# Performance work log

Measured on AMD Instinct MI355X. Metric: run time of the kernel, lower is better.

## Reference

```python
import jax, jax.numpy as jnp
import numpy as np

D_MODEL = 1536
NUM_EXPERTS = 64
TOP_K = 2
D_HIDDEN = 512
LN_EPS = 1e-5


def setup_inputs() -> dict:
    key = jax.random.key(0)
    ks = jax.random.split(key, 6)
    B, S = 2, 2048
    x = jax.random.normal(ks[0], (B, S, D_MODEL), dtype=jnp.float32)
    # router: nn.Linear(d_model, num_experts, bias=False) -> weight [E, D]
    Wr = jax.random.normal(ks[1], (NUM_EXPERTS, D_MODEL), dtype=jnp.float32) / np.sqrt(D_MODEL)
    # per-expert MLP weights, torch Linear layout: w1 [H, D], w2 [D, H], stacked over experts
    W1 = jax.random.normal(ks[2], (NUM_EXPERTS, D_HIDDEN, D_MODEL), dtype=jnp.float32) / np.sqrt(D_MODEL)
    W2 = jax.random.normal(ks[3], (NUM_EXPERTS, D_MODEL, D_HIDDEN), dtype=jnp.float32) / np.sqrt(D_HIDDEN)
    gamma = jnp.ones((D_MODEL,), dtype=jnp.float32)
    beta = jnp.zeros((D_MODEL,), dtype=jnp.float32)
    return {"x": x, "Wr": Wr, "W1": W1, "W2": W2, "gamma": gamma, "beta": beta}


def reference(x, Wr, W1, W2, gamma, beta):
    B, S, D = x.shape
    xf = x.reshape(-1, D)                                   # [T, D]
    logits = xf @ Wr.T                                      # [T, E]
    top_w, top_idx = jax.lax.top_k(logits, TOP_K)           # [T, K]
    top_w = jax.nn.softmax(top_w, axis=-1)                  # softmax over selected k
    # combine[t, e] = sum_k top_w[t, k] * 1{top_idx[t,k]==e}; zero for unselected experts,
    # so dense all-expert compute below is mathematically identical to the masked loop.
    onehot = jax.nn.one_hot(top_idx, NUM_EXPERTS, dtype=xf.dtype)   # [T, K, E]
    combine = jnp.einsum("tk,tke->te", top_w, onehot)       # [T, E]
    h = jax.nn.silu(jnp.einsum("td,ehd->teh", xf, W1))      # [T, E, H]
    hw = h * combine[:, :, None]                            # weight before second GEMM
    out = jnp.einsum("teh,edh->td", hw, W2)                 # [T, D]
    # LayerNorm (eps=1e-5, affine)
    mu = jnp.mean(out, axis=-1, keepdims=True)
    var = jnp.mean(jnp.square(out - mu), axis=-1, keepdims=True)
    out = (out - mu) * jax.lax.rsqrt(var + LN_EPS) * gamma + beta
    return out.reshape(B, S, D)
```

## Files before the change

### kernel.cpp

```cpp
#include <hip/hip_runtime.h>
#include <hip/hip_bf16.h>

#define D_MODEL 1536
#define NEXP    64
#define D_HID   512
#define NTOK    4096
#define NT1     (D_MODEL / 64)
#define NT2     (D_HID / 64)
#define MT      192

typedef __attribute__((ext_vector_type(8))) short short8;
typedef __attribute__((ext_vector_type(4))) float f32x4;

__device__ __forceinline__ unsigned short f2bf(float f) {
  unsigned u = __builtin_bit_cast(unsigned, f);
  u += 0x7FFFu + ((u >> 16) & 1u);
  return (unsigned short)(u >> 16);
}
__device__ __forceinline__ unsigned pk2(float a, float b) {
  return (unsigned)f2bf(a) | ((unsigned)f2bf(b) << 16);
}
__device__ __forceinline__ float bf2f(unsigned short u) {
  return __builtin_bit_cast(float, ((unsigned)u) << 16);
}

__device__ __forceinline__ void gl16(const void* g, void* s) {
  __builtin_amdgcn_global_load_lds(
      (const __attribute__((address_space(1))) unsigned int*)g,
      (__attribute__((address_space(3))) unsigned int*)s, 16, 0, 0);
}

#define WAITV(N)  asm volatile("s_waitcnt vmcnt(" #N ")" ::: "memory")
#define WAITL0    asm volatile("s_waitcnt lgkmcnt(0)" ::: "memory")
#define SBAR      __builtin_amdgcn_s_barrier()
#define SCHED0    __builtin_amdgcn_sched_barrier(0)


__global__ void zero_small_kernel(int* __restrict__ counts) {
  counts[threadIdx.x] = 0;
}


__global__ __launch_bounds__(256) void cvt_split_kernel(const float* __restrict__ x,
    const float* __restrict__ Wr,
    unsigned short* __restrict__ xhi, unsigned short* __restrict__ xlo,
    unsigned short* __restrict__ whi, unsigned short* __restrict__ wlo)
{
  const float* src; unsigned short* dhi; unsigned short* dlo; long i;
  long bid = blockIdx.x;
  if (bid < 3072) { src = x;  dhi = xhi; dlo = xlo; i = (bid * 256 + threadIdx.x) * 8; }
  else            { src = Wr; dhi = whi; dlo = wlo; i = ((bid - 3072) * 256 + threadIdx.x) * 8; }
  float4 a = *(const float4*)(src + i);
  float4 b = *(const float4*)(src + i + 4);
  float f[8] = {a.x, a.y, a.z, a.w, b.x, b.y, b.z, b.w};
  unsigned short h[8], l[8];
  #pragma unroll
  for (int j = 0; j < 8; ++j) {
    h[j] = f2bf(f[j]);
    l[j] = f2bf(f[j] - bf2f(h[j]));
  }
  uint4 ph, pl;
  ph.x = (unsigned)h[0] | ((unsigned)h[1] << 16);
  ph.y = (unsigned)h[2] | ((unsigned)h[3] << 16);
  ph.z = (unsigned)h[4] | ((unsigned)h[5] << 16);
  ph.w = (unsigned)h[6] | ((unsigned)h[7] << 16);
  pl.x = (unsigned)l[0] | ((unsigned)l[1] << 16);
  pl.y = (unsigned)l[2] | ((unsigned)l[3] << 16);
  pl.z = (unsigned)l[4] | ((unsigned)l[5] << 16);
  pl.w = (unsigned)l[6] | ((unsigned)l[7] << 16);
  *(uint4*)(dhi + i) = ph;
  *(uint4*)(dlo + i) = pl;
}


__global__ __launch_bounds__(256) void router_kernel(
    const unsigned short* __restrict__ xhi, const unsigned short* __restrict__ xlo,
    const unsigned short* __restrict__ whi, const unsigned short* __restrict__ wlo,
    int* __restrict__ topidx, float* __restrict__ topw, int* __restrict__ counts)
{
  __shared__ unsigned short lds[8 * 4096];
  const int tid  = threadIdx.x;
  const int lane = tid & 63;
  const int wv   = tid >> 6;
  const int t0   = blockIdx.x * 64;

  const int lslot = (lane & 7) ^ (lane >> 3);
  const unsigned short* gsrc[4][2];
  #pragma unroll
  for (int j = 0; j < 2; ++j) {
    int r = (wv * 2 + j) * 8 + (lane >> 3);
    gsrc[0][j] = xhi + (long)(t0 + r) * D_MODEL + lslot * 8;
    gsrc[1][j] = xlo + (long)(t0 + r) * D_MODEL + lslot * 8;
    gsrc[2][j] = whi + (long)r * D_MODEL + lslot * 8;
    gsrc[3][j] = wlo + (long)r * D_MODEL + lslot * 8;
  }

  auto ISSUE = [&](int t, int b) {
    const int k0 = t * 64;
    SCHED0;
    #pragma unroll
    for (int tile = 0; tile < 4; ++tile)
      #pragma unroll
      for (int j = 0; j < 2; ++j)
        gl16(gsrc[tile][j] + k0, &lds[(b * 4 + tile) * 4096 + (wv * 2 + j) * 512]);
    SCHED0;
  };

  f32x4 acc[4];
  #pragma unroll
  for (int i = 0; i < 4; ++i) acc[i] = (f32x4)0.f;

  const int arow = wv * 16 + (lane & 15);

  auto COMPUTE = [&](int b) {
    const unsigned short* Ah = &lds[(b * 4 + 0) * 4096];
    const unsigned short* Al = &lds[(b * 4 + 1) * 4096];
    const unsigned short* Bh = &lds[(b * 4 + 2) * 4096];
    const unsigned short* Bl = &lds[(b * 4 + 3) * 4096];
    #pragma unroll
    for (int ks = 0; ks < 2; ++ks) {
      int pa = (ks * 4 + (lane >> 4)) ^ (arow & 7);
      short8 ah = *(const short8*)(Ah + arow * 64 + pa * 8);
      short8 al = *(const short8*)(Al + arow * 64 + pa * 8);
      short8 bh[4], bl[4];
      #pragma unroll
      for (int ni = 0; ni < 4; ++ni) {
        int br = ni * 16 + (lane & 15);
        int pb = (ks * 4 + (lane >> 4)) ^ (br & 7);
        bh[ni] = *(const short8*)(Bh + br * 64 + pb * 8);
        bl[ni] = *(const short8*)(Bl + br * 64 + pb * 8);
      }
      __builtin_amdgcn_s_setprio(1);
      #pragma unroll
      for (int ni = 0; ni < 4; ++ni) {
        acc[ni] = __builtin_amdgcn_mfma_f32_16x16x32_bf16(ah, bh[ni], acc[ni], 0, 0, 0);
        acc[ni] = __builtin_amdgcn_mfma_f32_16x16x32_bf16(ah, bl[ni], acc[ni], 0, 0, 0);
        acc[ni] = __builtin_amdgcn_mfma_f32_16x16x32_bf16(al, bh[ni], acc[ni], 0, 0, 0);
      }
      __builtin_amdgcn_s_setprio(0);
    }
  };

  ISSUE(0, 0);
  ISSUE(1, 1);
  WAITV(8);
  SBAR;

  #pragma unroll 1
  for (int t = 0; t < NT1; t += 2) {
    COMPUTE(0);
    SBAR;
    if (t + 2 < NT1) { ISSUE(t + 2, 0); WAITV(8); }
    else             { WAITV(0); }
    SBAR;
    COMPUTE(1);
    SBAR;
    if (t + 2 < NT1) {
      if (t + 3 < NT1) { ISSUE(t + 3, 1); WAITV(8); }
      else             { WAITV(0); }
      SBAR;
    }
  }

  float* lgl = (float*)lds;
  #pragma unroll
  for (int ni = 0; ni < 4; ++ni)
    #pragma unroll
    for (int rg = 0; rg < 4; ++rg) {
      int tok = wv * 16 + (lane >> 4) * 4 + rg;
      int e   = ni * 16 + (lane & 15);
      lgl[tok * 66 + e] = acc[ni][rg];
    }
  __syncthreads();

  for (int i = 0; i < 16; ++i) {
    const int tl = wv * 16 + i;
    float v = lgl[tl * 66 + lane];
    float v0 = v; int e0 = lane;
    #pragma unroll
    for (int off = 32; off > 0; off >>= 1) {
      float ov = __shfl_xor(v0, off);
      int   oe = __shfl_xor(e0, off);
      if (ov > v0 || (ov == v0 && oe < e0)) { v0 = ov; e0 = oe; }
    }
    float v1 = (lane == e0) ? -3.0e38f : v;
    int e1 = lane;
    #pragma unroll
    for (int off = 32; off > 0; off >>= 1) {
      float ov = __shfl_xor(v1, off);
      int   oe = __shfl_xor(e1, off);
      if (ov > v1 || (ov == v1 && oe < e1)) { v1 = ov; e1 = oe; }
    }
    if (lane == 0) {
      int tt = t0 + tl;
      float w0 = 1.f / (1.f + expf(v1 - v0));
      topidx[tt * 2]     = e0;
      topidx[tt * 2 + 1] = e1;
      topw[tt * 2]       = w0;
      topw[tt * 2 + 1]   = 1.f - w0;
      atomicAdd(&counts[e0], 1);
      atomicAdd(&counts[e1], 1);
    }
  }
}


__global__ void scan_kernel(const int* __restrict__ counts, int* __restrict__ offs,
                            int* __restrict__ cursor)
{
  int e = threadIdx.x;
  int c = counts[e];
  int xx = c;
  #pragma unroll
  for (int off = 1; off < 64; off <<= 1) {
    int y = __shfl_up(xx, off);
    if (e >= off) xx += y;
  }
  offs[e + 1] = xx;
  if (e == 0) offs[0] = 0;
  cursor[e] = 0;
}

__global__ void scatter_kernel(const int* __restrict__ topidx, const float* __restrict__ topw,
    const int* __restrict__ offs, int* __restrict__ cursor,
    int* __restrict__ perm, float* __restrict__ wgt, int* __restrict__ tok2slot)
{
  int t = blockIdx.x * blockDim.x + threadIdx.x;
  if (t >= NTOK) return;
  #pragma unroll
  for (int k = 0; k < 2; ++k) {
    int e = topidx[t * 2 + k];
    float w = topw[t * 2 + k];
    int pos = atomicAdd(&cursor[e], 1);
    int slot = offs[e] + pos;
    perm[slot] = t;
    wgt[slot] = w;
    tok2slot[t * 2 + k] = slot;
  }
}

#define FS(T, AB, BRI, BRW, KNT)                                   \
  {                                                                \
    COMPUTE(Abuf[AB], Bbuf[AB]);                                   \
    SBAR;                                                          \
    if ((T) + 2 < (KNT)) ISSUEA((T) + 2, Abuf[AB]);                \
    if ((T) + 3 < (KNT)) ISSUEB((T) + 3, BRI);                     \
    if ((T) + 3 < (KNT))      { WAITV(14); }                       \
    else if ((T) + 2 < (KNT)) { WAITV(10); }                       \
    else                      { WAITV(0);  }                       \
    if ((T) + 1 < (KNT)) { WRITE_B(BRW, Bbuf[(AB) ^ 1]); WAITL0; } \
    SBAR;                                                          \
  }


__global__ __launch_bounds__(256, 2) void ffn1_kernel(
    const unsigned short* __restrict__ xb, const float* __restrict__ W1,
    const int* __restrict__ offs, const int* __restrict__ perm,
    const float* __restrict__ wgt, unsigned short* __restrict__ hbuf)
{
  const int bid = blockIdx.x;
  const int e   = (bid & 7) * 8 + (bid >> 6);
  const int nc  = (bid >> 3) & 7;
  const int cnt = offs[e + 1] - offs[e];
  if (cnt == 0) return;

  __shared__ unsigned short Abuf[2][MT * 64];
  __shared__ unsigned short Bbuf[2][64 * 64];

  const int tid  = threadIdx.x;
  const int lane = tid & 63;
  const int wv   = tid >> 6;

  const int qB = tid & 15;
  const int rB = tid >> 4;
  const float* bptr[4];
  #pragma unroll
  for (int p = 0; p < 4; ++p)
    bptr[p] = W1 + ((long)e * D_HID + nc * 64 + p * 16 + rB) * D_MODEL + qB * 4;

  int arow[3], brow[4];
  int physA[2][3], physB[2][4];
  #pragma unroll
  for (int mi = 0; mi < 3; ++mi) {
    arow[mi] = wv * 48 + mi * 16 + (lane & 15);
    #pragma unroll
    for (int ks = 0; ks < 2; ++ks)
      physA[ks][mi] = (ks * 4 + (lane >> 4)) ^ (arow[mi] & 7);
  }
  #pragma unroll
  for (int ni = 0; ni < 4; ++ni) {
    brow[ni] = ni * 16 + (lane & 15);
    #pragma unroll
    for (int ks = 0; ks < 2; ++ks)
      physB[ks][ni] = (ks * 4 + (lane >> 4)) ^ (brow[ni] & 7);
  }
  const int lslot = (lane & 7) ^ (lane >> 3);

  for (int m0 = 0; m0 < cnt; m0 += MT) {
    const int base = offs[e] + m0;
    const int mcnt = min(MT, cnt - m0);

    const unsigned short* gptrA[6];
    #pragma unroll
    for (int j = 0; j < 6; ++j) {
      int pr = (wv * 6 + j) * 8 + (lane >> 3);
      if (pr >= mcnt) pr = mcnt - 1;
      gptrA[j] = xb + (long)perm[base + pr] * D_MODEL + lslot * 8;
    }

    f32x4 acc[3][4];
    #pragma unroll
    for (int i = 0; i < 3; ++i)
      #pragma unroll
      for (int j = 0; j < 4; ++j) acc[i][j] = (f32x4)0.f;

    float4 br0[4], br1[4], br2[4];

    auto ISSUEA = [&](int t, unsigned short* Ab) {
      const int k0 = t * 64;
      SCHED0;
      #pragma unroll
      for (int j = 0; j < 6; ++j)
        gl16(gptrA[j] + k0, Ab + (wv * 6 + j) * 512);
      SCHED0;
    };
    auto ISSUEB = [&](int t, float4* br) {
      const int k0 = t * 64;
      SCHED0;
      #pragma unroll
      for (int p = 0; p < 4; ++p) br[p] = *(const float4*)(bptr[p] + k0);
      SCHED0;
    };
    auto WRITE_B = [&](const float4* br, unsigned short* B_) {
      #pragma unroll
      for (int p = 0; p < 4; ++p) {
        int rr = p * 16 + rB;
        unsigned lo = pk2(br[p].x, br[p].y);
        unsigned hi = pk2(br[p].z, br[p].w);
        int ph = (qB >> 1) ^ (rr & 7);
        *(uint2*)(B_ + rr * 64 + ph * 8 + (qB & 1) * 4) = make_uint2(lo, hi);
      }
    };
    auto COMPUTE = [&](const unsigned short* A_, const unsigned short* B_) {
      #pragma unroll
      for (int ks = 0; ks < 2; ++ks) {
        short8 a[3], bb[4];
        #pragma unroll
        for (int mi = 0; mi < 3; ++mi)
          a[mi] = *(const short8*)(A_ + arow[mi] * 64 + physA[ks][mi] * 8);
        #pragma unroll
        for (int ni = 0; ni < 4; ++ni)
          bb[ni] = *(const short8*)(B_ + brow[ni] * 64 + physB[ks][ni] * 8);
        __builtin_amdgcn_s_setprio(1);
        #pragma unroll
        for (int mi = 0; mi < 3; ++mi)
          #pragma unroll
          for (int ni = 0; ni < 4; ++ni)
            acc[mi][ni] = __builtin_amdgcn_mfma_f32_16x16x32_bf16(a[mi], bb[ni], acc[mi][ni], 0, 0, 0);
        __builtin_amdgcn_s_setprio(0);
      }
    };

    ISSUEA(0, Abuf[0]); ISSUEB(0, br0);
    ISSUEA(1, Abuf[1]); ISSUEB(1, br1);
    ISSUEB(2, br2);
    WAITV(14);
    WRITE_B(br0, Bbuf[0]);
    WAITL0;
    SBAR;

    #pragma unroll 1
    for (int t = 0; t < NT1; t += 6) {
      FS(t + 0, 0, br0, br1, NT1);
      FS(t + 1, 1, br1, br2, NT1);
      FS(t + 2, 0, br2, br0, NT1);
      FS(t + 3, 1, br0, br1, NT1);
      FS(t + 4, 0, br1, br2, NT1);
      FS(t + 5, 1, br2, br0, NT1);
    }

    unsigned short* fds = &Abuf[0][0];
    const int rsub = (lane >> 4) * 4;
    const int csub = lane & 15;
    #pragma unroll
    for (int mi = 0; mi < 3; ++mi) {
      #pragma unroll
      for (int rg = 0; rg < 4; ++rg) {
        int r = wv * 48 + mi * 16 + rsub + rg;
        float wt = (r < mcnt) ? wgt[base + r] : 0.f;
        #pragma unroll
        for (int ni = 0; ni < 4; ++ni) {
          float v = acc[mi][ni][rg];
          float sv = v / (1.f + __expf(-v)) * wt;
          fds[r * 64 + ni * 16 + csub] = f2bf(sv);
        }
      }
    }
    __syncthreads();
    #pragma unroll
    for (int q = 0; q < 6; ++q) {
      int idx = q * 256 + tid;
      int row = idx >> 3, c8 = idx & 7;
      if (row < mcnt)
        *(uint4*)(hbuf + (long)(base + row) * D_HID + nc * 64 + c8 * 8) =
            *(const uint4*)(fds + row * 64 + c8 * 8);
    }
    __syncthreads();
  }
}


__global__ __launch_bounds__(256, 2) void ffn2_kernel(
    const unsigned short* __restrict__ hbuf, const float* __restrict__ W2,
    const int* __restrict__ offs, unsigned short* __restrict__ sbuf)
{
  const int bid = blockIdx.x;
  const int j   = bid >> 3;
  const int e   = (bid & 7) * 8 + j / 24;
  const int nc  = j % 24;
  const int cnt = offs[e + 1] - offs[e];
  if (cnt == 0) return;

  __shared__ unsigned short Abuf[2][MT * 64];
  __shared__ unsigned short Bbuf[2][64 * 64];

  const int tid  = threadIdx.x;
  const int lane = tid & 63;
  const int wv   = tid >> 6;

  const int qB = tid & 15;
  const int rB = tid >> 4;
  const float* bptr[4];
  #pragma unroll
  for (int p = 0; p < 4; ++p)
    bptr[p] = W2 + ((long)e * D_MODEL + nc * 64 + p * 16 + rB) * D_HID + qB * 4;

  int arow[3], brow[4];
  int physA[2][3], physB[2][4];
  #pragma unroll
  for (int mi = 0; mi < 3; ++mi) {
    arow[mi] = wv * 48 + mi * 16 + (lane & 15);
    #pragma unroll
    for (int ks = 0; ks < 2; ++ks)
      physA[ks][mi] = (ks * 4 + (lane >> 4)) ^ (arow[mi] & 7);
  }
  #pragma unroll
  for (int ni = 0; ni < 4; ++ni) {
    brow[ni] = ni * 16 + (lane & 15);
    #pragma unroll
    for (int ks = 0; ks < 2; ++ks)
      physB[ks][ni] = (ks * 4 + (lane >> 4)) ^ (brow[ni] & 7);
  }
  const int lslot = (lane & 7) ^ (lane >> 3);

  for (int m0 = 0; m0 < cnt; m0 += MT) {
    const int base = offs[e] + m0;
    const int mcnt = min(MT, cnt - m0);

    const unsigned short* gptrA[6];
    #pragma unroll
    for (int j2 = 0; j2 < 6; ++j2) {
      int pr = (wv * 6 + j2) * 8 + (lane >> 3);
      if (pr >= mcnt) pr = mcnt - 1;
      gptrA[j2] = hbuf + (long)(base + pr) * D_HID + lslot * 8;
    }

    f32x4 acc[3][4];
    #pragma unroll
    for (int i = 0; i < 3; ++i)
      #pragma unroll
      for (int j2 = 0; j2 < 4; ++j2) acc[i][j2] = (f32x4)0.f;

    float4 br0[4], br1[4], br2[4];

    auto ISSUEA = [&](int t, unsigned short* Ab) {
      const int k0 = t * 64;
      SCHED0;
      #pragma unroll
      for (int j2 = 0; j2 < 6; ++j2)
        gl16(gptrA[j2] + k0, Ab + (wv * 6 + j2) * 512);
      SCHED0;
    };
    auto ISSUEB = [&](int t, float4* br) {
      const int k0 = t * 64;
      SCHED0;
      #pragma unroll
      for (int p = 0; p < 4; ++p) br[p] = *(const float4*)(bptr[p] + k0);
      SCHED0;
    };
    auto WRITE_B = [&](const float4* br, unsigned short* B_) {
      #pragma unroll
      for (int p = 0; p < 4; ++p) {
        int rr = p * 16 + rB;
        unsigned lo = pk2(br[p].x, br[p].y);
        unsigned hi = pk2(br[p].z, br[p].w);
        int ph = (qB >> 1) ^ (rr & 7);
        *(uint2*)(B_ + rr * 64 + ph * 8 + (qB & 1) * 4) = make_uint2(lo, hi);
      }
    };
    auto COMPUTE = [&](const unsigned short* A_, const unsigned short* B_) {
      #pragma unroll
      for (int ks = 0; ks < 2; ++ks) {
        short8 a[3], bb[4];
        #pragma unroll
        for (int mi = 0; mi < 3; ++mi)
          a[mi] = *(const short8*)(A_ + arow[mi] * 64 + physA[ks][mi] * 8);
        #pragma unroll
        for (int ni = 0; ni < 4; ++ni)
          bb[ni] = *(const short8*)(B_ + brow[ni] * 64 + physB[ks][ni] * 8);
        __builtin_amdgcn_s_setprio(1);
        #pragma unroll
        for (int mi = 0; mi < 3; ++mi)
          #pragma unroll
          for (int ni = 0; ni < 4; ++ni)
            acc[mi][ni] = __builtin_amdgcn_mfma_f32_16x16x32_bf16(a[mi], bb[ni], acc[mi][ni], 0, 0, 0);
        __builtin_amdgcn_s_setprio(0);
      }
    };

    ISSUEA(0, Abuf[0]); ISSUEB(0, br0);
    ISSUEA(1, Abuf[1]); ISSUEB(1, br1);
    ISSUEB(2, br2);
    WAITV(14);
    WRITE_B(br0, Bbuf[0]);
    WAITL0;
    SBAR;

    FS(0, 0, br0, br1, NT2);
    FS(1, 1, br1, br2, NT2);
    FS(2, 0, br2, br0, NT2);
    FS(3, 1, br0, br1, NT2);
    FS(4, 0, br1, br2, NT2);
    FS(5, 1, br2, br0, NT2);
    FS(6, 0, br0, br1, NT2);
    FS(7, 1, br1, br2, NT2);

    unsigned short* fds = &Abuf[0][0];
    const int rsub = (lane >> 4) * 4;
    const int csub = lane & 15;
    #pragma unroll
    for (int mi = 0; mi < 3; ++mi) {
      #pragma unroll
      for (int rg = 0; rg < 4; ++rg) {
        int r = wv * 48 + mi * 16 + rsub + rg;
        #pragma unroll
        for (int ni = 0; ni < 4; ++ni)
          fds[r * 64 + ni * 16 + csub] = f2bf(acc[mi][ni][rg]);
      }
    }
    __syncthreads();
    #pragma unroll
    for (int q = 0; q < 6; ++q) {
      int idx = q * 256 + tid;
      int row = idx >> 3, c8 = idx & 7;
      if (row < mcnt)
        *(uint4*)(sbuf + (long)(base + row) * D_MODEL + nc * 64 + c8 * 8) =
            *(const uint4*)(fds + row * 64 + c8 * 8);
    }
    __syncthreads();
  }
}


__global__ __launch_bounds__(192) void ln_kernel(const unsigned short* __restrict__ sbuf,
    const int* __restrict__ tok2slot, float* __restrict__ out,
    const float* __restrict__ gamma, const float* __restrict__ beta)
{
  const int tid = threadIdx.x;
  const int t = blockIdx.x;
  const long r0 = (long)tok2slot[t * 2]     * D_MODEL;
  const long r1 = (long)tok2slot[t * 2 + 1] * D_MODEL;

  uint4 u0 = *(const uint4*)(sbuf + r0 + tid * 8);
  uint4 u1 = *(const uint4*)(sbuf + r1 + tid * 8);
  float v[8];
  {
    const unsigned* p0 = &u0.x;
    const unsigned* p1 = &u1.x;
    #pragma unroll
    for (int i = 0; i < 4; ++i) {
      v[i * 2]     = bf2f((unsigned short)(p0[i] & 0xFFFFu)) + bf2f((unsigned short)(p1[i] & 0xFFFFu));
      v[i * 2 + 1] = bf2f((unsigned short)(p0[i] >> 16))     + bf2f((unsigned short)(p1[i] >> 16));
    }
  }

  float s = 0.f, sq = 0.f;
  #pragma unroll
  for (int i = 0; i < 8; ++i) { s += v[i]; sq += v[i] * v[i]; }
  #pragma unroll
  for (int off = 32; off > 0; off >>= 1) {
    s  += __shfl_xor(s, off);
    sq += __shfl_xor(sq, off);
  }
  __shared__ float ss[3], sqs[3];
  int wv = tid >> 6;
  if ((tid & 63) == 0) { ss[wv] = s; sqs[wv] = sq; }
  __syncthreads();
  s  = ss[0] + ss[1] + ss[2];
  sq = sqs[0] + sqs[1] + sqs[2];
  const float inv = 1.f / (float)D_MODEL;
  float mu  = s * inv;
  float var = sq * inv - mu * mu;
  float rs  = 1.f / sqrtf(var + 1e-5f);

  float4 g1 = *(const float4*)(gamma + tid * 8);
  float4 g2 = *(const float4*)(gamma + tid * 8 + 4);
  float4 b1v = *(const float4*)(beta + tid * 8);
  float4 b2v = *(const float4*)(beta + tid * 8 + 4);
  float4 a, b;
  a.x = (v[0] - mu) * rs * g1.x + b1v.x;
  a.y = (v[1] - mu) * rs * g1.y + b1v.y;
  a.z = (v[2] - mu) * rs * g1.z + b1v.z;
  a.w = (v[3] - mu) * rs * g1.w + b1v.w;
  b.x = (v[4] - mu) * rs * g2.x + b2v.x;
  b.y = (v[5] - mu) * rs * g2.y + b2v.y;
  b.z = (v[6] - mu) * rs * g2.z + b2v.z;
  b.w = (v[7] - mu) * rs * g2.w + b2v.w;
  float* row = out + (long)t * D_MODEL;
  *(float4*)(row + tid * 8)     = a;
  *(float4*)(row + tid * 8 + 4) = b;
}


extern "C" void kernel_launch(void* const* d_in, const int* in_sizes, int n_in,
                              void* d_out, int out_size, void* d_ws, size_t ws_size,
                              hipStream_t stream) {
  const float* x     = (const float*)d_in[0];
  const float* Wr    = (const float*)d_in[1];
  const float* W1    = (const float*)d_in[2];
  const float* W2    = (const float*)d_in[3];
  const float* gamma = (const float*)d_in[4];
  const float* beta  = (const float*)d_in[5];
  float* out = (float*)d_out;

  char* ws = (char*)d_ws;
  unsigned short* xhi    = (unsigned short*)(ws + 0);
  unsigned short* xlo    = (unsigned short*)(ws + 12582912);
  unsigned short* hbuf   = (unsigned short*)(ws + 25165824);
  unsigned short* sbuf   = (unsigned short*)(ws + 33554432);
  unsigned short* whi    = (unsigned short*)(ws + 58720256);
  unsigned short* wlo    = (unsigned short*)(ws + 58916864);
  int*   topidx   = (int*)  (ws + 59113472);
  float* topw     = (float*)(ws + 59146240);
  int*   counts   = (int*)  (ws + 59179008);
  int*   cursor   = (int*)  (ws + 59179264);
  int*   offs     = (int*)  (ws + 59179520);
  int*   tok2slot = (int*)  (ws + 59180032);
  int*   perm     = (int*)  (ws + 59212800);
  float* wgt      = (float*)(ws + 59245568);

  hipLaunchKernelGGL(zero_small_kernel, dim3(1), dim3(64), 0, stream, counts);
  hipLaunchKernelGGL(cvt_split_kernel, dim3(3120), dim3(256), 0, stream, x, Wr, xhi, xlo, whi, wlo);
  hipLaunchKernelGGL(router_kernel, dim3(NTOK / 64), dim3(256), 0, stream, xhi, xlo, whi, wlo, topidx, topw, counts);
  hipLaunchKernelGGL(scan_kernel, dim3(1), dim3(64), 0, stream, counts, offs, cursor);
  hipLaunchKernelGGL(scatter_kernel, dim3(NTOK / 256), dim3(256), 0, stream, topidx, topw, offs, cursor, perm, wgt, tok2slot);
  hipLaunchKernelGGL(ffn1_kernel, dim3(512), dim3(256), 0, stream, xhi, W1, offs, perm, wgt, hbuf);
  hipLaunchKernelGGL(ffn2_kernel, dim3(1536), dim3(256), 0, stream, hbuf, W2, offs, sbuf);
  hipLaunchKernelGGL(ln_kernel, dim3(NTOK), dim3(192), 0, stream, sbuf, tok2slot, out, gamma, beta);
}
```

Measured before the change: 223.1 us.

## Split MFMA k-steps to interleave B-tile LDS write mid-compute

Splits each tile's compute into two k-substeps and moves the conversion and LDS write of the next B tile between them, so the bf16 packing and LDS stores overlap with MFMA work instead of running after the barrier. It removes the scheduling barriers and priority hints around loads and MFMAs, and reorders the prologue so B for tile 1 is issued before A for tile 1, which changes the vmcnt wait counts. The changes touch both expert GEMM kernels. The risk is an incorrect vmcnt accounting or less precise instruction scheduling now that the sched barriers and setprio are gone.

```diff
diff --git a/kernel.cpp b/kernel.cpp
--- a/kernel.cpp
+++ b/kernel.cpp
@@ -239,17 +239,22 @@
   }
 }
 
-#define FS(T, AB, BRI, BRW, KNT)                                   \
-  {                                                                \
-    COMPUTE(Abuf[AB], Bbuf[AB]);                                   \
-    SBAR;                                                          \
-    if ((T) + 2 < (KNT)) ISSUEA((T) + 2, Abuf[AB]);                \
-    if ((T) + 3 < (KNT)) ISSUEB((T) + 3, BRI);                     \
-    if ((T) + 3 < (KNT))      { WAITV(14); }                       \
-    else if ((T) + 2 < (KNT)) { WAITV(10); }                       \
-    else                      { WAITV(0);  }                       \
-    if ((T) + 1 < (KNT)) { WRITE_B(BRW, Bbuf[(AB) ^ 1]); WAITL0; } \
-    SBAR;                                                          \
+#define FS(T, AB, BRI, BRW, KNT)                                    \
+  {                                                                 \
+    CKS(Abuf[AB], Bbuf[AB], 0);                                     \
+    if ((T) + 1 < (KNT)) {                                          \
+      if ((T) + 2 < (KNT)) { WAITV(10); } else { WAITV(6); }        \
+      WRITE_B(BRW, Bbuf[(AB) ^ 1]);                                 \
+    }                                                               \
+    CKS(Abuf[AB], Bbuf[AB], 1);                                     \
+    SBAR;                                                           \
+    if ((T) + 2 < (KNT)) ISSUEA((T) + 2, Abuf[AB]);                 \
+    if ((T) + 3 < (KNT)) ISSUEB((T) + 3, BRI);                      \
+    if ((T) + 3 < (KNT))      { WAITV(14); }                        \
+    else if ((T) + 2 < (KNT)) { WAITV(10); }                        \
+    else                      { WAITV(0);  }                        \
+    WAITL0;                                                         \
+    SBAR;                                                           \
   }
 
 
@@ -318,18 +323,14 @@
 
     auto ISSUEA = [&](int t, unsigned short* Ab) {
       const int k0 = t * 64;
-      SCHED0;
       #pragma unroll
       for (int j = 0; j < 6; ++j)
         gl16(gptrA[j] + k0, Ab + (wv * 6 + j) * 512);
-      SCHED0;
     };
     auto ISSUEB = [&](int t, float4* br) {
       const int k0 = t * 64;
-      SCHED0;
       #pragma unroll
       for (int p = 0; p < 4; ++p) br[p] = *(const float4*)(bptr[p] + k0);
-      SCHED0;
     };
     auto WRITE_B = [&](const float4* br, unsigned short* B_) {
       #pragma unroll
@@ -341,29 +342,24 @@
         *(uint2*)(B_ + rr * 64 + ph * 8 + (qB & 1) * 4) = make_uint2(lo, hi);
       }
     };
-    auto COMPUTE = [&](const unsigned short* A_, const unsigned short* B_) {
-      #pragma unroll
-      for (int ks = 0; ks < 2; ++ks) {
-        short8 a[3], bb[4];
-        #pragma unroll
-        for (int mi = 0; mi < 3; ++mi)
-          a[mi] = *(const short8*)(A_ + arow[mi] * 64 + physA[ks][mi] * 8);
+    auto CKS = [&](const unsigned short* A_, const unsigned short* B_, int ks) {
+      short8 a[3], bb[4];
+      #pragma unroll
+      for (int mi = 0; mi < 3; ++mi)
+        a[mi] = *(const short8*)(A_ + arow[mi] * 64 + physA[ks][mi] * 8);
+      #pragma unroll
+      for (int ni = 0; ni < 4; ++ni)
+        bb[ni] = *(const short8*)(B_ + brow[ni] * 64 + physB[ks][ni] * 8);
+      #pragma unroll
+      for (int mi = 0; mi < 3; ++mi)
         #pragma unroll
         for (int ni = 0; ni < 4; ++ni)
-          bb[ni] = *(const short8*)(B_ + brow[ni] * 64 + physB[ks][ni] * 8);
-        __builtin_amdgcn_s_setprio(1);
-        #pragma unroll
-        for (int mi = 0; mi < 3; ++mi)
-          #pragma unroll
-          for (int ni = 0; ni < 4; ++ni)
-            acc[mi][ni] = __builtin_amdgcn_mfma_f32_16x16x32_bf16(a[mi], bb[ni], acc[mi][ni], 0, 0, 0);
-        __builtin_amdgcn_s_setprio(0);
-      }
+          acc[mi][ni] = __builtin_amdgcn_mfma_f32_16x16x32_bf16(a[mi], bb[ni], acc[mi][ni], 0, 0, 0);
     };
 
     ISSUEA(0, Abuf[0]); ISSUEB(0, br0);
-    ISSUEA(1, Abuf[1]); ISSUEB(1, br1);
-    ISSUEB(2, br2);
+    ISSUEB(1, br1);
+    ISSUEA(1, Abuf[1]); ISSUEB(2, br2);
     WAITV(14);
     WRITE_B(br0, Bbuf[0]);
     WAITL0;
@@ -475,18 +471,14 @@
 
     auto ISSUEA = [&](int t, unsigned short* Ab) {
       const int k0 = t * 64;
-      SCHED0;
       #pragma unroll
       for (int j2 = 0; j2 < 6; ++j2)
         gl16(gptrA[j2] + k0, Ab + (wv * 6 + j2) * 512);
-      SCHED0;
     };
     auto ISSUEB = [&](int t, float4* br) {
       const int k0 = t * 64;
-      SCHED0;
       #pragma unroll
       for (int p = 0; p < 4; ++p) br[p] = *(const float4*)(bptr[p] + k0);
-      SCHED0;
     };
     auto WRITE_B = [&](const float4* br, unsigned short* B_) {
       #pragma unroll
@@ -498,29 +490,24 @@
         *(uint2*)(B_ + rr * 64 + ph * 8 + (qB & 1) * 4) = make_uint2(lo, hi);
       }
     };
-    auto COMPUTE = [&](const unsigned short* A_, const unsigned short* B_) {
-      #pragma unroll
-      for (int ks = 0; ks < 2; ++ks) {
-        short8 a[3], bb[4];
-        #pragma unroll
-        for (int mi = 0; mi < 3; ++mi)
-          a[mi] = *(const short8*)(A_ + arow[mi] * 64 + physA[ks][mi] * 8);
+    auto CKS = [&](const unsigned short* A_, const unsigned short* B_, int ks) {
+      short8 a[3], bb[4];
+      #pragma unroll
+      for (int mi = 0; mi < 3; ++mi)
+        a[mi] = *(const short8*)(A_ + arow[mi] * 64 + physA[ks][mi] * 8);
+      #pragma unroll
+      for (int ni = 0; ni < 4; ++ni)
+        bb[ni] = *(const short8*)(B_ + brow[ni] * 64 + physB[ks][ni] * 8);
+      #pragma unroll
+      for (int mi = 0; mi < 3; ++mi)
         #pragma unroll
         for (int ni = 0; ni < 4; ++ni)
-          bb[ni] = *(const short8*)(B_ + brow[ni] * 64 + physB[ks][ni] * 8);
-        __builtin_amdgcn_s_setprio(1);
-        #pragma unroll
-        for (int mi = 0; mi < 3; ++mi)
-          #pragma unroll
-          for (int ni = 0; ni < 4; ++ni)
-            acc[mi][ni] = __builtin_amdgcn_mfma_f32_16x16x32_bf16(a[mi], bb[ni], acc[mi][ni], 0, 0, 0);
-        __builtin_amdgcn_s_setprio(0);
-      }
+          acc[mi][ni] = __builtin_amdgcn_mfma_f32_16x16x32_bf16(a[mi], bb[ni], acc[mi][ni], 0, 0, 0);
     };
 
     ISSUEA(0, Abuf[0]); ISSUEB(0, br0);
-    ISSUEA(1, Abuf[1]); ISSUEB(1, br1);
-    ISSUEB(2, br2);
+    ISSUEB(1, br1);
+    ISSUEA(1, Abuf[1]); ISSUEB(2, br2);
     WAITV(14);
     WRITE_B(br0, Bbuf[0]);
     WAITL0;
```

New measurement: 215.2 us. 3.5% less time.
